# Kernel tuning notes

Hardware: AMD Instinct MI355X
Metric: run time of the kernel (lower is better)

The kernel has to match this reference:

```python
import jax, jax.numpy as jnp
import numpy as np

K = 2  # top-k experts per token


def setup_inputs() -> dict:
    key = jax.random.key(0)
    k1, k2 = jax.random.split(key)
    B, T, D, E = 4, 4096, 4096, 64
    x = jax.random.normal(k1, (B, T, D), dtype=jnp.float32)
    W = jax.random.normal(k2, (E, D), dtype=jnp.float32) * (1.0 / np.sqrt(D))
    return {"x": x, "W": W}


def reference(x, W):
    # router_logits: [B, T, E]  (nn.Linear with no bias: x @ W.T)
    router_logits = jnp.einsum('btd,ed->bte', x, W)
    # top-k over expert dim, then softmax over the k selected logits
    topk_logits, topk_idx = jax.lax.top_k(router_logits, K)  # [B,T,K]
    topk_weight = jax.nn.softmax(topk_logits, axis=-1)       # [B,T,K]
    return (topk_idx, topk_weight, router_logits)
```

## Files before the change

kernel.cpp:

```cpp
#include <hip/hip_runtime.h>
#include <math.h>

#define NTOK 16384
#define DDIM 4096
#define NEXP 64
#define TAU  2e-4f
#define WS_LO 262144
#define NCW  32

typedef short bf16x8 __attribute__((ext_vector_type(8)));
typedef float f32x4  __attribute__((ext_vector_type(4)));

__device__ __forceinline__ unsigned short bf16_rne(float f) {
  unsigned u = __float_as_uint(f);
  u += 0x7fffu + ((u >> 16) & 1u);
  return (unsigned short)(u >> 16);
}

__device__ __forceinline__ void split4(float4 v, uint2& hi, uint2& lo) {
  unsigned h0 = bf16_rne(v.x), h1 = bf16_rne(v.y), h2 = bf16_rne(v.z), h3 = bf16_rne(v.w);
  float r0 = v.x - __uint_as_float(h0 << 16);
  float r1 = v.y - __uint_as_float(h1 << 16);
  float r2 = v.z - __uint_as_float(h2 << 16);
  float r3 = v.w - __uint_as_float(h3 << 16);
  unsigned l0 = bf16_rne(r0), l1 = bf16_rne(r1), l2 = bf16_rne(r2), l3 = bf16_rne(r3);
  hi = make_uint2(h0 | (h1 << 16), h2 | (h3 << 16));
  lo = make_uint2(l0 | (l1 << 16), l2 | (l3 << 16));
}

__device__ __forceinline__ void split4v(f32x4 v, uint2& hi, uint2& lo) {
  unsigned h0 = bf16_rne(v[0]), h1 = bf16_rne(v[1]), h2 = bf16_rne(v[2]), h3 = bf16_rne(v[3]);
  float r0 = v[0] - __uint_as_float(h0 << 16);
  float r1 = v[1] - __uint_as_float(h1 << 16);
  float r2 = v[2] - __uint_as_float(h2 << 16);
  float r3 = v[3] - __uint_as_float(h3 << 16);
  unsigned l0 = bf16_rne(r0), l1 = bf16_rne(r1), l2 = bf16_rne(r2), l3 = bf16_rne(r3);
  hi = make_uint2(h0 | (h1 << 16), h2 | (h3 << 16));
  lo = make_uint2(l0 | (l1 << 16), l2 | (l3 << 16));
}

__device__ __forceinline__ bf16x8 mk8(uint2 a, uint2 b) {
  union { uint4 u; bf16x8 v; } t;
  t.u = make_uint4(a.x, a.y, b.x, b.y);
  return t.v;
}

__device__ __forceinline__ void gld_lds16(const float* g, char* l) {
  __builtin_amdgcn_global_load_lds((const __attribute__((address_space(1))) void*)g,
                                   (__attribute__((address_space(3))) void*)l,
                                   16, 0, 0);
}

__device__ __forceinline__ bool better(float va, int ia, float vb, int ib) {
  return (va > vb) || (va == vb && ia < ib);
}
__device__ __forceinline__ bool betterd(double va, int ia, double vb, int ib) {
  return (va > vb) || (va == vb && ia < ib);
}
#define CE(va, ia, vb, ib) { if (better(vb, ib, va, ia)) { float _tv = va; va = vb; vb = _tv; int _ti = ia; ia = ib; ib = _ti; } }

__global__ __launch_bounds__(256)
void presplit_w(const float* __restrict__ w, short* __restrict__ ws) {
  const int tid = blockIdx.x * 256 + threadIdx.x;
  const int e = tid >> 9;
  const int o = tid & 511;
  const int c = o >> 2, q = o & 3;
  const int l = (e & 15) + 16 * q;
  const int g = e >> 4;
  const float* src = w + (size_t)e * DDIM + o * 8;
  float4 v0 = *(const float4*)src;
  float4 v1 = *(const float4*)(src + 4);
  uint2 h0, s0, h1, s1;
  split4(v0, h0, s0);
  split4(v1, h1, s1);
  const int off = c * 2048 + g * 512 + l * 8;
  *(uint4*)(ws + off)         = make_uint4(h0.x, h0.y, h1.x, h1.y);
  *(uint4*)(ws + WS_LO + off) = make_uint4(s0.x, s0.y, s1.x, s1.y);
}

__device__ __noinline__ void fixup_token(const float* __restrict__ x,
                                         const float* __restrict__ wgt,
                                         float* __restrict__ out_idx,
                                         float* __restrict__ out_wt,
                                         int tok, unsigned pk, int l) {
  const int e0 = pk & 255, e1 = (pk >> 8) & 255, e2 = (pk >> 16) & 255, e3 = (pk >> 24) & 255;
  const float* xr = x   + (size_t)tok * DDIM + l * 64;
  const float* w0 = wgt + (size_t)e0 * DDIM + l * 64;
  const float* w1 = wgt + (size_t)e1 * DDIM + l * 64;
  const float* w2 = wgt + (size_t)e2 * DDIM + l * 64;
  const float* w3 = wgt + (size_t)e3 * DDIM + l * 64;
  double s0 = 0.0, s1 = 0.0, s2 = 0.0, s3 = 0.0;
#pragma unroll 4
  for (int j = 0; j < 64; j += 4) {
    float4 xv = *(const float4*)(xr + j);
    float4 av = *(const float4*)(w0 + j);
    s0 = fma((double)xv.x, (double)av.x, s0); s0 = fma((double)xv.y, (double)av.y, s0);
    s0 = fma((double)xv.z, (double)av.z, s0); s0 = fma((double)xv.w, (double)av.w, s0);
    av = *(const float4*)(w1 + j);
    s1 = fma((double)xv.x, (double)av.x, s1); s1 = fma((double)xv.y, (double)av.y, s1);
    s1 = fma((double)xv.z, (double)av.z, s1); s1 = fma((double)xv.w, (double)av.w, s1);
    av = *(const float4*)(w2 + j);
    s2 = fma((double)xv.x, (double)av.x, s2); s2 = fma((double)xv.y, (double)av.y, s2);
    s2 = fma((double)xv.z, (double)av.z, s2); s2 = fma((double)xv.w, (double)av.w, s2);
    av = *(const float4*)(w3 + j);
    s3 = fma((double)xv.x, (double)av.x, s3); s3 = fma((double)xv.y, (double)av.y, s3);
    s3 = fma((double)xv.z, (double)av.z, s3); s3 = fma((double)xv.w, (double)av.w, s3);
  }
#pragma unroll
  for (int m = 1; m < 64; m <<= 1) {
    s0 += __shfl_xor(s0, m);
    s1 += __shfl_xor(s1, m);
    s2 += __shfl_xor(s2, m);
    s3 += __shfl_xor(s3, m);
  }
  if (l == 0) {
    double v0 = s0, v1 = s1, v2 = s2, v3 = s3;
    int i0 = e0, i1 = e1, i2 = e2, i3 = e3;
    if (betterd(v1, i1, v0, i0)) { double tv = v0; v0 = v1; v1 = tv; int ti = i0; i0 = i1; i1 = ti; }
    if (betterd(v3, i3, v2, i2)) { double tv = v2; v2 = v3; v3 = tv; int ti = i2; i2 = i3; i3 = ti; }
    if (betterd(v2, i2, v0, i0)) { double tv = v0; v0 = v2; v2 = tv; int ti = i0; i0 = i2; i2 = ti; }
    if (betterd(v3, i3, v1, i1)) { double tv = v1; v1 = v3; v3 = tv; int ti = i1; i1 = i3; i3 = ti; }
    if (betterd(v2, i2, v1, i1)) { double tv = v1; v1 = v2; v2 = tv; int ti = i1; i1 = i2; i2 = ti; }
    double ex = exp(v1 - v0);
    double den = 1.0 + ex;
    out_idx[tok * 2 + 0] = (float)i0;
    out_idx[tok * 2 + 1] = (float)i1;
    out_wt[tok * 2 + 0]  = (float)(1.0 / den);
    out_wt[tok * 2 + 1]  = (float)(ex / den);
  }
}

__global__ __launch_bounds__(256, 2)
void router_main(const float* __restrict__ x, const float* __restrict__ wgt,
                 const short* __restrict__ ws, float* __restrict__ out) {
  __shared__ __align__(16) char ldsbuf[65536];

  const int u = threadIdx.x;
  const int l = u & 63;
  const int wid = u >> 6;
  const int tokBase = blockIdx.x * 64;

  char* ring = ldsbuf + wid * 16384;
  const unsigned ldsbase =
      (unsigned)(size_t)(__attribute__((address_space(3))) char*)&ldsbuf[0];
  const unsigned rbase = ldsbase + wid * 16384 + l * 16;

  const int P = (blockIdx.x * 13) & 31;
#define PHYS(T) (((T) + P) & 31)

  const float* xA0 = x + (size_t)(tokBase +  0 + (l & 15)) * DDIM + wid * 1024 + (l >> 4) * 8;
  const float* xB0 = xA0 + 4;
  const float* xA1 = x + (size_t)(tokBase + 16 + (l & 15)) * DDIM + wid * 1024 + (l >> 4) * 8;
  const float* xB1 = xA1 + 4;
  const float* xA2 = x + (size_t)(tokBase + 32 + (l & 15)) * DDIM + wid * 1024 + (l >> 4) * 8;
  const float* xB2 = xA2 + 4;
  const float* xA3 = x + (size_t)(tokBase + 48 + (l & 15)) * DDIM + wid * 1024 + (l >> 4) * 8;
  const float* xB3 = xA3 + 4;

  const short* wch = ws + wid * 65536 + l * 8;

  f32x4 acc[4][4];
#pragma unroll
  for (int t2 = 0; t2 < 4; ++t2)
#pragma unroll
    for (int g = 0; g < 4; ++g) acc[t2][g] = (f32x4){0.f, 0.f, 0.f, 0.f};

  bf16x8 wset[2][8];

#define LDW(SET, T)                                                            \
  { const int cw_ = ((T) < NCW) ? (T) : NCW - 1;                               \
    const int cc_ = PHYS(cw_);                                                 \
    asm volatile("" ::: "memory");                                             \
    wset[SET][0] = *(const bf16x8*)(wch + cc_ * 2048 + 0 * 512);               \
    wset[SET][1] = *(const bf16x8*)(wch + WS_LO + cc_ * 2048 + 0 * 512);       \
    wset[SET][2] = *(const bf16x8*)(wch + cc_ * 2048 + 1 * 512);               \
    wset[SET][3] = *(const bf16x8*)(wch + WS_LO + cc_ * 2048 + 1 * 512);       \
    wset[SET][4] = *(const bf16x8*)(wch + cc_ * 2048 + 2 * 512);               \
    wset[SET][5] = *(const bf16x8*)(wch + WS_LO + cc_ * 2048 + 2 * 512);       \
    wset[SET][6] = *(const bf16x8*)(wch + cc_ * 2048 + 3 * 512);               \
    wset[SET][7] = *(const bf16x8*)(wch + WS_LO + cc_ * 2048 + 3 * 512);       \
    asm volatile("" ::: "memory"); }

#define XISSUE(T, SLOT)                                                        \
  { const int cx_ = ((T) < NCW) ? (T) : NCW - 1;                               \
    const int cp_ = PHYS(cx_) * 32;                                            \
    char* d_ = ring + (SLOT) * 8192;                                           \
    gld_lds16(xA0 + cp_, d_);                                                  \
    gld_lds16(xB0 + cp_, d_ + 1024);                                           \
    gld_lds16(xA1 + cp_, d_ + 2048);                                           \
    gld_lds16(xB1 + cp_, d_ + 3072);                                           \
    gld_lds16(xA2 + cp_, d_ + 4096);                                           \
    gld_lds16(xB2 + cp_, d_ + 5120);                                           \
    gld_lds16(xA3 + cp_, d_ + 6144);                                           \
    gld_lds16(xB3 + cp_, d_ + 7168); }

#define MM(T2, G, SET)                                                         \
  acc[T2][G] = __builtin_amdgcn_mfma_f32_16x16x32_bf16(ahi, wset[SET][2*(G)],   acc[T2][G], 0, 0, 0); \
  acc[T2][G] = __builtin_amdgcn_mfma_f32_16x16x32_bf16(ahi, wset[SET][2*(G)+1], acc[T2][G], 0, 0, 0); \
  acc[T2][G] = __builtin_amdgcn_mfma_f32_16x16x32_bf16(alo, wset[SET][2*(G)],   acc[T2][G], 0, 0, 0);

#define COMPT(T2, SET, F0, F1)                                                 \
  { uint2 h0_, s0_, h1_, s1_;                                                  \
    split4v(F0, h0_, s0_); split4v(F1, h1_, s1_);                              \
    bf16x8 ahi = mk8(h0_, h1_), alo = mk8(s0_, s1_);                           \
    MM(T2, 0, SET) MM(T2, 1, SET) MM(T2, 2, SET) MM(T2, 3, SET) }

#define STEP(T, SLOT, SET)                                                     \
  {                                                                            \
    asm volatile("s_waitcnt vmcnt(16)" ::: "memory");                          \
    f32x4 f0, f1, f2, f3, f4, f5, f6, f7;                                      \
    { unsigned a_ = rbase + (SLOT) * 8192;                                     \
      asm volatile("ds_read_b128 %0, %2\n\tds_read_b128 %1, %2 offset:1024"    \
                   : "=&v"(f0), "=&v"(f1) : "v"(a_));                          \
      asm volatile("ds_read_b128 %0, %2 offset:2048\n\tds_read_b128 %1, %2 offset:3072" \
                   : "=&v"(f2), "=&v"(f3) : "v"(a_));                          \
      asm volatile("ds_read_b128 %0, %2 offset:4096\n\tds_read_b128 %1, %2 offset:5120" \
                   : "=&v"(f4), "=&v"(f5) : "v"(a_));                          \
      asm volatile("ds_read_b128 %0, %2 offset:6144\n\tds_read_b128 %1, %2 offset:7168" \
                   : "=&v"(f6), "=&v"(f7) : "v"(a_)); }                        \
    asm volatile("s_waitcnt lgkmcnt(0)" ::: "memory");                         \
    __builtin_amdgcn_sched_barrier(0);                                         \
    XISSUE((T) + 2, SLOT)                                                      \
    asm volatile("" ::: "memory");                                             \
    COMPT(0, SET, f0, f1)                                                      \
    COMPT(1, SET, f2, f3)                                                      \
    COMPT(2, SET, f4, f5)                                                      \
    COMPT(3, SET, f6, f7)                                                      \
    LDW(SET, (T) + 2)                                                          \
  }

  XISSUE(0, 0)
  LDW(0, 0)
  XISSUE(1, 1)
  LDW(1, 1)

  for (int t = 0; t < NCW; t += 2) {
    STEP(t, 0, 0)
    STEP(t + 1, 1, 1)
  }

  __syncthreads();
  float* p = (float*)ldsbuf;
#define PIDX(KQ, T2, G, R) ((((((KQ) * 4 + (T2)) * 4 + (G)) * 4 + (R)) << 6) + l)
#pragma unroll
  for (int t2 = 0; t2 < 4; ++t2)
#pragma unroll
    for (int g = 0; g < 4; ++g)
#pragma unroll
      for (int r = 0; r < 4; ++r)
        p[PIDX(wid, t2, g, r)] = acc[t2][g][r];
  __syncthreads();

  float* out_idx = out;
  float* out_wt  = out + NTOK * 2;
  float* out_lg  = out + NTOK * 4;

#pragma unroll
  for (int t2 = 0; t2 < 4; ++t2) {
    float v0 = p[PIDX(0, t2, 0, wid)] + p[PIDX(1, t2, 0, wid)] + p[PIDX(2, t2, 0, wid)] + p[PIDX(3, t2, 0, wid)];
    float v1 = p[PIDX(0, t2, 1, wid)] + p[PIDX(1, t2, 1, wid)] + p[PIDX(2, t2, 1, wid)] + p[PIDX(3, t2, 1, wid)];
    float v2 = p[PIDX(0, t2, 2, wid)] + p[PIDX(1, t2, 2, wid)] + p[PIDX(2, t2, 2, wid)] + p[PIDX(3, t2, 2, wid)];
    float v3 = p[PIDX(0, t2, 3, wid)] + p[PIDX(1, t2, 3, wid)] + p[PIDX(2, t2, 3, wid)] + p[PIDX(3, t2, 3, wid)];

    const int tok = tokBase + t2 * 16 + (l >> 4) * 4 + wid;
    {
      float* dst = out_lg + (size_t)tok * NEXP + (l & 15);
      dst[0]  = v0;
      dst[16] = v1;
      dst[32] = v2;
      dst[48] = v3;
    }

    const int cbase = (l & 15);
    int i0 = cbase, i1 = cbase + 16, i2 = cbase + 32, i3 = cbase + 48;
    CE(v0, i0, v1, i1) CE(v2, i2, v3, i3) CE(v0, i0, v2, i2) CE(v1, i1, v3, i3) CE(v1, i1, v2, i2)
#pragma unroll
    for (int m = 1; m <= 8; m <<= 1) {
      float p0 = __shfl_xor(v0, m), p1 = __shfl_xor(v1, m);
      float p2 = __shfl_xor(v2, m), p3 = __shfl_xor(v3, m);
      int j0 = __shfl_xor(i0, m), j1 = __shfl_xor(i1, m);
      int j2 = __shfl_xor(i2, m), j3 = __shfl_xor(i3, m);
      CE(v0, i0, p3, j3) CE(v1, i1, p2, j2) CE(v2, i2, p1, j1) CE(v3, i3, p0, j0)
      CE(v0, i0, v2, i2) CE(v1, i1, v3, i3) CE(v0, i0, v1, i1) CE(v2, i2, v3, i3)
    }

    bool flag = false;
    unsigned pk = 0;
    if (cbase == 0) {
      flag = (v0 - v1 < TAU) || (v1 - v2 < TAU) || (v2 - v3 < TAU);
      pk = (unsigned)i0 | ((unsigned)i1 << 8) | ((unsigned)i2 << 16) | ((unsigned)i3 << 24);
      if (!flag) {
        float ex = expf(v1 - v0);
        float den = 1.0f + ex;
        out_idx[tok * 2 + 0] = (float)i0;
        out_idx[tok * 2 + 1] = (float)i1;
        out_wt[tok * 2 + 0]  = 1.0f / den;
        out_wt[tok * 2 + 1]  = ex / den;
      }
    }
    unsigned long long mk = __ballot(flag);
    while (mk) {
      const int src = __builtin_ctzll(mk);
      mk &= mk - 1;
      const unsigned pks = (unsigned)__shfl((int)pk, src);
      fixup_token(x, wgt, out_idx, out_wt, tokBase + t2 * 16 + (src >> 4) * 4 + wid, pks, l);
    }
  }
}

extern "C" void kernel_launch(void* const* d_in, const int* in_sizes, int n_in,
                              void* d_out, int out_size, void* d_ws, size_t ws_size,
                              hipStream_t stream) {
  const float* x = (const float*)d_in[0];
  const float* w = (const float*)d_in[1];
  float* out = (float*)d_out;
  short* ws = (short*)d_ws;

  hipLaunchKernelGGL(presplit_w, dim3(128), dim3(256), 0, stream, w, ws);
  hipLaunchKernelGGL(router_main, dim3(NTOK / 64), dim3(256), 0, stream, x, w, ws, out);
}
```

Measured before the change: 91.29 us.

## Halve tokens per block and split K across eight waves instead of four

```diff
diff --git a/kernel.cpp b/kernel.cpp
--- a/kernel.cpp
+++ b/kernel.cpp
@@ -6,7 +6,7 @@
 #define NEXP 64
 #define TAU  2e-4f
 #define WS_LO 262144
-#define NCW  32
+#define NCW  16
 
 typedef short bf16x8 __attribute__((ext_vector_type(8)));
 typedef float f32x4  __attribute__((ext_vector_type(4)));
@@ -130,7 +130,7 @@
   }
 }
 
-__global__ __launch_bounds__(256, 2)
+__global__ __launch_bounds__(512, 3)
 void router_main(const float* __restrict__ x, const float* __restrict__ wgt,
                  const short* __restrict__ ws, float* __restrict__ out) {
   __shared__ __align__(16) char ldsbuf[65536];
@@ -138,30 +138,26 @@
   const int u = threadIdx.x;
   const int l = u & 63;
   const int wid = u >> 6;
-  const int tokBase = blockIdx.x * 64;
-
-  char* ring = ldsbuf + wid * 16384;
+  const int tokBase = blockIdx.x * 32;
+
+  char* ring = ldsbuf + wid * 8192;
   const unsigned ldsbase =
       (unsigned)(size_t)(__attribute__((address_space(3))) char*)&ldsbuf[0];
-  const unsigned rbase = ldsbase + wid * 16384 + l * 16;
-
-  const int P = (blockIdx.x * 13) & 31;
-#define PHYS(T) (((T) + P) & 31)
-
-  const float* xA0 = x + (size_t)(tokBase +  0 + (l & 15)) * DDIM + wid * 1024 + (l >> 4) * 8;
+  const unsigned rbase = ldsbase + wid * 8192 + l * 16;
+
+  const int P = (blockIdx.x * 5) & 15;
+#define PHYS(T) (((T) + P) & 15)
+
+  const float* xA0 = x + (size_t)(tokBase +  0 + (l & 15)) * DDIM + wid * 512 + (l >> 4) * 8;
   const float* xB0 = xA0 + 4;
-  const float* xA1 = x + (size_t)(tokBase + 16 + (l & 15)) * DDIM + wid * 1024 + (l >> 4) * 8;
+  const float* xA1 = x + (size_t)(tokBase + 16 + (l & 15)) * DDIM + wid * 512 + (l >> 4) * 8;
   const float* xB1 = xA1 + 4;
-  const float* xA2 = x + (size_t)(tokBase + 32 + (l & 15)) * DDIM + wid * 1024 + (l >> 4) * 8;
-  const float* xB2 = xA2 + 4;
-  const float* xA3 = x + (size_t)(tokBase + 48 + (l & 15)) * DDIM + wid * 1024 + (l >> 4) * 8;
-  const float* xB3 = xA3 + 4;
-
-  const short* wch = ws + wid * 65536 + l * 8;
-
-  f32x4 acc[4][4];
-#pragma unroll
-  for (int t2 = 0; t2 < 4; ++t2)
+
+  const short* wch = ws + wid * 32768 + l * 8;
+
+  f32x4 acc[2][4];
+#pragma unroll
+  for (int t2 = 0; t2 < 2; ++t2)
 #pragma unroll
     for (int g = 0; g < 4; ++g) acc[t2][g] = (f32x4){0.f, 0.f, 0.f, 0.f};
 
@@ -184,15 +180,11 @@
 #define XISSUE(T, SLOT)                                                        \
   { const int cx_ = ((T) < NCW) ? (T) : NCW - 1;                               \
     const int cp_ = PHYS(cx_) * 32;                                            \
-    char* d_ = ring + (SLOT) * 8192;                                           \
+    char* d_ = ring + (SLOT) * 4096;                                           \
     gld_lds16(xA0 + cp_, d_);                                                  \
     gld_lds16(xB0 + cp_, d_ + 1024);                                           \
     gld_lds16(xA1 + cp_, d_ + 2048);                                           \
-    gld_lds16(xB1 + cp_, d_ + 3072);                                           \
-    gld_lds16(xA2 + cp_, d_ + 4096);                                           \
-    gld_lds16(xB2 + cp_, d_ + 5120);                                           \
-    gld_lds16(xA3 + cp_, d_ + 6144);                                           \
-    gld_lds16(xB3 + cp_, d_ + 7168); }
+    gld_lds16(xB1 + cp_, d_ + 3072); }
 
 #define MM(T2, G, SET)                                                         \
   acc[T2][G] = __builtin_amdgcn_mfma_f32_16x16x32_bf16(ahi, wset[SET][2*(G)],   acc[T2][G], 0, 0, 0); \
@@ -207,25 +199,19 @@
 
 #define STEP(T, SLOT, SET)                                                     \
   {                                                                            \
-    asm volatile("s_waitcnt vmcnt(16)" ::: "memory");                          \
-    f32x4 f0, f1, f2, f3, f4, f5, f6, f7;                                      \
-    { unsigned a_ = rbase + (SLOT) * 8192;                                     \
+    asm volatile("s_waitcnt vmcnt(12)" ::: "memory");                          \
+    f32x4 f0, f1, f2, f3;                                                      \
+    { unsigned a_ = rbase + (SLOT) * 4096;                                     \
       asm volatile("ds_read_b128 %0, %2\n\tds_read_b128 %1, %2 offset:1024"    \
                    : "=&v"(f0), "=&v"(f1) : "v"(a_));                          \
       asm volatile("ds_read_b128 %0, %2 offset:2048\n\tds_read_b128 %1, %2 offset:3072" \
-                   : "=&v"(f2), "=&v"(f3) : "v"(a_));                          \
-      asm volatile("ds_read_b128 %0, %2 offset:4096\n\tds_read_b128 %1, %2 offset:5120" \
-                   : "=&v"(f4), "=&v"(f5) : "v"(a_));                          \
-      asm volatile("ds_read_b128 %0, %2 offset:6144\n\tds_read_b128 %1, %2 offset:7168" \
-                   : "=&v"(f6), "=&v"(f7) : "v"(a_)); }                        \
+                   : "=&v"(f2), "=&v"(f3) : "v"(a_)); }                        \
     asm volatile("s_waitcnt lgkmcnt(0)" ::: "memory");                         \
     __builtin_amdgcn_sched_barrier(0);                                         \
     XISSUE((T) + 2, SLOT)                                                      \
     asm volatile("" ::: "memory");                                             \
     COMPT(0, SET, f0, f1)                                                      \
     COMPT(1, SET, f2, f3)                                                      \
-    COMPT(2, SET, f4, f5)                                                      \
-    COMPT(3, SET, f6, f7)                                                      \
     LDW(SET, (T) + 2)                                                          \
   }
 
@@ -241,9 +227,9 @@
 
   __syncthreads();
   float* p = (float*)ldsbuf;
-#define PIDX(KQ, T2, G, R) ((((((KQ) * 4 + (T2)) * 4 + (G)) * 4 + (R)) << 6) + l)
-#pragma unroll
-  for (int t2 = 0; t2 < 4; ++t2)
+#define PIDX(KQ, T2, G, R) ((((((KQ) * 2 + (T2)) * 4 + (G)) * 4 + (R)) << 6) + l)
+#pragma unroll
+  for (int t2 = 0; t2 < 2; ++t2)
 #pragma unroll
     for (int g = 0; g < 4; ++g)
 #pragma unroll
@@ -255,14 +241,19 @@
   float* out_wt  = out + NTOK * 2;
   float* out_lg  = out + NTOK * 4;
 
-#pragma unroll
-  for (int t2 = 0; t2 < 4; ++t2) {
-    float v0 = p[PIDX(0, t2, 0, wid)] + p[PIDX(1, t2, 0, wid)] + p[PIDX(2, t2, 0, wid)] + p[PIDX(3, t2, 0, wid)];
-    float v1 = p[PIDX(0, t2, 1, wid)] + p[PIDX(1, t2, 1, wid)] + p[PIDX(2, t2, 1, wid)] + p[PIDX(3, t2, 1, wid)];
-    float v2 = p[PIDX(0, t2, 2, wid)] + p[PIDX(1, t2, 2, wid)] + p[PIDX(2, t2, 2, wid)] + p[PIDX(3, t2, 2, wid)];
-    float v3 = p[PIDX(0, t2, 3, wid)] + p[PIDX(1, t2, 3, wid)] + p[PIDX(2, t2, 3, wid)] + p[PIDX(3, t2, 3, wid)];
-
-    const int tok = tokBase + t2 * 16 + (l >> 4) * 4 + wid;
+  {
+    const int t2 = wid >> 2;
+    const int r  = wid & 3;
+    float v0 = 0.f, v1 = 0.f, v2 = 0.f, v3 = 0.f;
+#pragma unroll
+    for (int kq = 0; kq < 8; ++kq) {
+      v0 += p[PIDX(kq, t2, 0, r)];
+      v1 += p[PIDX(kq, t2, 1, r)];
+      v2 += p[PIDX(kq, t2, 2, r)];
+      v3 += p[PIDX(kq, t2, 3, r)];
+    }
+
+    const int tok = tokBase + t2 * 16 + (l >> 4) * 4 + r;
     {
       float* dst = out_lg + (size_t)tok * NEXP + (l & 15);
       dst[0]  = v0;
@@ -303,7 +294,7 @@
       const int src = __builtin_ctzll(mk);
       mk &= mk - 1;
       const unsigned pks = (unsigned)__shfl((int)pk, src);
-      fixup_token(x, wgt, out_idx, out_wt, tokBase + t2 * 16 + (src >> 4) * 4 + wid, pks, l);
+      fixup_token(x, wgt, out_idx, out_wt, tokBase + t2 * 16 + (src >> 4) * 4 + r, pks, l);
     }
   }
 }
@@ -317,5 +308,5 @@
   short* ws = (short*)d_ws;
 
   hipLaunchKernelGGL(presplit_w, dim3(128), dim3(256), 0, stream, w, ws);
-  hipLaunchKernelGGL(router_main, dim3(NTOK / 64), dim3(256), 0, stream, x, w, ws, out);
-}
+  hipLaunchKernelGGL(router_main, dim3(NTOK / 32), dim3(512), 0, stream, x, w, ws, out);
+}
```

Measured after the change: 91.49 us. About the same (+0.2%).
